# Kernel tuning notes

Measured on AMD Instinct MI355X. Metric: run time of the kernel, lower is better.

The kernel has to match this reference:

```python
import jax, jax.numpy as jnp
import numpy as np

N_NODES = 100000
N_EDGES = 1600000
D_IN, D_HID, D_OUT = 128, 128, 64


def gcn_conv(x, src, dst, deg_inv_sqrt, W, b, n_nodes):
    # PyG GCNConv (normalize=True, add_self_loops already folded into src/dst/deg):
    # out = scatter_add( d^{-1/2}[src] * d^{-1/2}[dst] * (x @ W)[src] ) + b
    h = x @ W                                    # [N, d_out]
    norm = deg_inv_sqrt[src] * deg_inv_sqrt[dst]  # [E+N]
    msg = h[src] * norm[:, None]                  # [E+N, d_out] (edge gather)
    out = jax.ops.segment_sum(msg, dst, num_segments=n_nodes)
    return out + b


def _augment(edge_index, n_nodes):
    # add self-loops and compute symmetric-normalization degrees (in-degree at dst)
    loop = jnp.arange(n_nodes, dtype=edge_index.dtype)
    src = jnp.concatenate([edge_index[0], loop])
    dst = jnp.concatenate([edge_index[1], loop])
    deg = jax.ops.segment_sum(jnp.ones_like(dst, dtype=jnp.float32), dst,
                              num_segments=n_nodes)
    deg_inv_sqrt = jnp.where(deg > 0, jax.lax.rsqrt(jnp.maximum(deg, 1.0)), 0.0)
    return src, dst, deg_inv_sqrt


def setup_inputs() -> dict:
    key = jax.random.key(0)
    k1, k2, k3, k4 = jax.random.split(key, 4)
    x = jax.random.normal(k1, (N_NODES, D_IN), dtype=jnp.float32)
    edge_index = jax.random.randint(k2, (2, N_EDGES), 0, N_NODES, dtype=jnp.int32)
    s = 1.0 / np.sqrt(D_IN)
    W1 = jax.random.uniform(k3, (D_IN, D_HID), dtype=jnp.float32, minval=-s, maxval=s)
    b1 = jnp.zeros((D_HID,), dtype=jnp.float32)
    s2 = 1.0 / np.sqrt(D_HID)
    W2 = jax.random.uniform(k4, (D_HID, D_OUT), dtype=jnp.float32, minval=-s2, maxval=s2)
    b2 = jnp.zeros((D_OUT,), dtype=jnp.float32)
    return {"x": x, "edge_index": edge_index, "W1": W1, "b1": b1, "W2": W2, "b2": b2}


def reference(x, edge_index, W1, b1, W2, b2):
    n_nodes = x.shape[0]
    src, dst, dinv = _augment(edge_index, n_nodes)
    h = gcn_conv(x, src, dst, dinv, W1, b1, n_nodes)
    h = jax.nn.relu(h)
    # dropout is identity in eval mode (F.dropout with training=False)
    out = gcn_conv(h, src, dst, dinv, W2, b2, n_nodes)
    return out
```

## Files before the change

kernel.cpp:

```cpp
#include <hip/hip_runtime.h>

typedef unsigned int uint;
typedef unsigned short ushort;
typedef __attribute__((ext_vector_type(8))) short short8v;
typedef __attribute__((ext_vector_type(4))) float f32x4;

#define NBMAX 512
#define BSHIFT 8

__device__ __forceinline__ ushort f2bf(float f) {
    uint u = __float_as_uint(f);
    u += 0x7fffu + ((u >> 16) & 1u);
    return (ushort)(u >> 16);
}


__global__ void bucket_hist(const int* __restrict__ dst, int* __restrict__ bcnt,
                            int E, int nbk) {
    __shared__ int s[NBMAX];
    int t = threadIdx.x;
    for (int i = t; i < nbk; i += 256) s[i] = 0;
    __syncthreads();
    int i0 = blockIdx.x * 4096 + t;
#pragma unroll
    for (int k = 0; k < 16; ++k) {
        int i = i0 + k * 256;
        if (i < E) atomicAdd(&s[dst[i] >> BSHIFT], 1);
    }
    __syncthreads();
    for (int i = t; i < nbk; i += 256) if (s[i] > 0) atomicAdd(&bcnt[i], s[i]);
}

__global__ void bucket_scan(const int* __restrict__ bcnt, int* __restrict__ bstart,
                            int* __restrict__ bcur, int nbk) {
    __shared__ int s[512];
    int t = threadIdx.x;
    int v = (t < nbk) ? bcnt[t] : 0;
    s[t] = v;
    __syncthreads();
    for (int o = 1; o < 512; o <<= 1) {
        int tv = (t >= o) ? s[t - o] : 0;
        __syncthreads();
        s[t] += tv;
        __syncthreads();
    }
    if (t < nbk) {
        int ex = s[t] - v;
        bstart[t] = ex;
        bcur[t] = ex;
    }
}

__global__ void bucket_scatter(const int* __restrict__ src, const int* __restrict__ dst,
                               int* __restrict__ bcur, int* __restrict__ tsw, int E) {
    __shared__ int cnt[NBMAX];
    __shared__ int base[NBMAX];
    int t = threadIdx.x;
    for (int i = t; i < NBMAX; i += 256) cnt[i] = 0;
    __syncthreads();
    int i0 = blockIdx.x * 4096 + t;
    int p_[16], b_[16], r_[16];
#pragma unroll
    for (int k = 0; k < 16; ++k) {
        int i = i0 + k * 256;
        if (i < E) {
            int s = src[i], d = dst[i];
            int bb = d >> BSHIFT;
            b_[k] = bb;
            p_[k] = s | ((d & ((1 << BSHIFT) - 1)) << 17);
            r_[k] = atomicAdd(&cnt[bb], 1);
        } else {
            b_[k] = -1;
        }
    }
    __syncthreads();
    for (int i = t; i < NBMAX; i += 256) if (cnt[i] > 0) base[i] = atomicAdd(&bcur[i], cnt[i]);
    __syncthreads();
#pragma unroll
    for (int k = 0; k < 16; ++k) {
        if (b_[k] >= 0) {
            int p = base[b_[k]] + r_[k];
            tsw[p] = p_[k];
        }
    }
}

__global__ void sort_bucket(const int* __restrict__ tsw, const int* __restrict__ bstart,
                            float* __restrict__ dinv, int* __restrict__ rp,
                            int* __restrict__ edata, int N, int E, int nbk) {
    __shared__ int cnt[256];
    __shared__ int cursor[256];
    int b = blockIdx.x;
    int t = threadIdx.x;
    int estart = bstart[b];
    int eend = (b + 1 < nbk) ? bstart[b + 1] : E;

    cnt[t] = 0;
    __syncthreads();
    for (int i = estart + t; i < eend; i += 256) {
        atomicAdd(&cnt[(uint)tsw[i] >> 17], 1);
    }
    __syncthreads();

    int node = (b << BSHIFT) + t;
    int self = (node < N) ? 1 : 0;
    int deg = cnt[t];
    int v = deg + self;
    cursor[t] = v;
    __syncthreads();
    for (int o = 1; o < 256; o <<= 1) {
        int tv = (t >= o) ? cursor[t - o] : 0;
        __syncthreads();
        cursor[t] += tv;
        __syncthreads();
    }
    int ex = cursor[t] - v;
    int gbase = estart + (b << BSHIFT);

    if (node < N) {
        dinv[node] = rsqrtf((float)(deg + 1));
        rp[node] = gbase + ex;
        edata[gbase + ex] = node;
    }
    if (b == nbk - 1 && t == 0) rp[N] = E + N;
    cursor[t] = ex + self;
    __syncthreads();

    for (int i = estart + t; i < eend; i += 256) {
        uint rec = (uint)tsw[i];
        int pos = gbase + atomicAdd(&cursor[rec >> 17], 1);
        edata[pos] = (int)(rec & 0x1FFFFu);
    }
}

__global__ void zero_row(ushort* __restrict__ Hz, int len) {
    int i = threadIdx.x;
    if (i < len) Hz[i] = 0;
}


__global__ void prep_w(const float* __restrict__ W1, const float* __restrict__ W2,
                       ushort* __restrict__ Wt1s, ushort* __restrict__ Wt2s) {
    int t = blockIdx.x * 256 + threadIdx.x;
    int total = gridDim.x * 256;
    for (int idx = t; idx < 128 * 128; idx += total) {
        int nn = idx >> 7, kk = idx & 127;
        uint byte = (uint)nn * 256u + (uint)kk * 2u;
        byte ^= (uint)((nn & 7) << 4);
        Wt1s[byte >> 1] = f2bf(W1[kk * 128 + nn]);
    }
    for (int idx = t; idx < 64 * 128; idx += total) {
        int nn = idx >> 7, kk = idx & 127;
        uint byte = (uint)nn * 256u + (uint)kk * 2u;
        byte ^= (uint)((nn & 7) << 4);
        Wt2s[byte >> 1] = f2bf(W2[kk * 64 + nn]);
    }
}


template <int NCOLS, bool IN_BF16>
__launch_bounds__(256)
__global__ void gemm_mfma(const void* __restrict__ Xv, const ushort* __restrict__ Wimg,
                          ushort* __restrict__ H, const float* __restrict__ dinv, int n) {
    constexpr int NT = NCOLS / 16;
    __shared__ ushort sW[NCOLS * 128];
    {
        const uint4* src = (const uint4*)Wimg;
        uint4* dst = (uint4*)sW;
        constexpr int NV = NCOLS * 128 * 2 / 16;
        for (int i = threadIdx.x; i < NV; i += 256) dst[i] = src[i];
    }
    __syncthreads();

    const int w  = threadIdx.x >> 6;
    const int l  = threadIdx.x & 63;
    const int lm = l & 15, lk = l >> 4;
    const int row_base = blockIdx.x * 128 + w * 32;

    f32x4 acc[2][NT];
#pragma unroll
    for (int mt = 0; mt < 2; ++mt)
#pragma unroll
        for (int nt = 0; nt < NT; ++nt) {
            f32x4 z = {0.f, 0.f, 0.f, 0.f};
            acc[mt][nt] = z;
        }

    int r0 = row_base + lm;
    int r1 = row_base + 16 + lm;
    int r0c = r0 < n ? r0 : n - 1;
    int r1c = r1 < n ? r1 : n - 1;

#pragma unroll
    for (int kb = 0; kb < 4; ++kb) {
        short8v a0, a1;
        if constexpr (IN_BF16) {
            const ushort* X = (const ushort*)Xv;
            a0 = *(const short8v*)(X + (size_t)r0c * 128 + kb * 32 + lk * 8);
            a1 = *(const short8v*)(X + (size_t)r1c * 128 + kb * 32 + lk * 8);
        } else {
            const float* X = (const float*)Xv;
            const float* p0 = X + (size_t)r0c * 128 + kb * 32 + lk * 8;
            const float* p1 = X + (size_t)r1c * 128 + kb * 32 + lk * 8;
            float4 u0 = *(const float4*)p0;
            float4 v0 = *(const float4*)(p0 + 4);
            float4 u1 = *(const float4*)p1;
            float4 v1 = *(const float4*)(p1 + 4);
            a0[0] = (short)f2bf(u0.x); a0[1] = (short)f2bf(u0.y);
            a0[2] = (short)f2bf(u0.z); a0[3] = (short)f2bf(u0.w);
            a0[4] = (short)f2bf(v0.x); a0[5] = (short)f2bf(v0.y);
            a0[6] = (short)f2bf(v0.z); a0[7] = (short)f2bf(v0.w);
            a1[0] = (short)f2bf(u1.x); a1[1] = (short)f2bf(u1.y);
            a1[2] = (short)f2bf(u1.z); a1[3] = (short)f2bf(u1.w);
            a1[4] = (short)f2bf(v1.x); a1[5] = (short)f2bf(v1.y);
            a1[6] = (short)f2bf(v1.z); a1[7] = (short)f2bf(v1.w);
        }
#pragma unroll
        for (int nt = 0; nt < NT; ++nt) {
            int nn = nt * 16 + lm;
            uint byte = (uint)nn * 256u + (uint)kb * 64u + (uint)lk * 16u;
            byte ^= (uint)((nn & 7) << 4);
            short8v b = *(const short8v*)((const char*)sW + byte);
            acc[0][nt] = __builtin_amdgcn_mfma_f32_16x16x32_bf16(a0, b, acc[0][nt], 0, 0, 0);
            acc[1][nt] = __builtin_amdgcn_mfma_f32_16x16x32_bf16(a1, b, acc[1][nt], 0, 0, 0);
        }
    }

    float dvs[2][4];
#pragma unroll
    for (int mt = 0; mt < 2; ++mt)
#pragma unroll
        for (int r = 0; r < 4; ++r) {
            int row = row_base + mt * 16 + lk * 4 + r;
            dvs[mt][r] = (row < n) ? dinv[row] : 0.f;
        }
#pragma unroll
    for (int mt = 0; mt < 2; ++mt)
#pragma unroll
        for (int nt = 0; nt < NT; ++nt)
#pragma unroll
            for (int r = 0; r < 4; ++r) {
                int row = row_base + mt * 16 + lk * 4 + r;
                if (row < n) H[(size_t)row * NCOLS + nt * 16 + lm] = f2bf(acc[mt][nt][r] * dvs[mt][r]);
            }
}


template <bool RELU>
__launch_bounds__(256)
__global__ void agg128(const ushort* __restrict__ H, const int* __restrict__ rp,
                       const int* __restrict__ edata, const float* __restrict__ dinv,
                       const float* __restrict__ bias, ushort* __restrict__ out, int N) {
    int gw = (blockIdx.x * 256 + threadIdx.x) >> 6;
    int lane = threadIdx.x & 63;
    if (gw >= N) return;
    const int h = lane >> 5, c = lane & 31;
    int e = rp[gw], end = rp[gw + 1];
    float a0 = 0.f, a1 = 0.f, a2 = 0.f, a3 = 0.f;

    for (; e < end; e += 32) {
        int md = N;
        if (lane < 32 && e + lane < end) md = edata[e + lane];
#pragma unroll
        for (int j = 0; j < 16; ++j) {
            int si = __shfl(md, 2 * j + h);
            uint2 hv = *(const uint2*)&H[(size_t)si * 128 + c * 4];
            a0 += __uint_as_float(hv.x << 16);
            a1 += __uint_as_float(hv.x & 0xffff0000u);
            a2 += __uint_as_float(hv.y << 16);
            a3 += __uint_as_float(hv.y & 0xffff0000u);
        }
    }
    a0 += __shfl_xor(a0, 32); a1 += __shfl_xor(a1, 32);
    a2 += __shfl_xor(a2, 32); a3 += __shfl_xor(a3, 32);
    if (h == 0) {
        float dg = dinv[gw];
        float4 bv = *(const float4*)&bias[c * 4];
        a0 = dg * a0 + bv.x; a1 = dg * a1 + bv.y;
        a2 = dg * a2 + bv.z; a3 = dg * a3 + bv.w;
        if (RELU) {
            a0 = fmaxf(a0, 0.f); a1 = fmaxf(a1, 0.f);
            a2 = fmaxf(a2, 0.f); a3 = fmaxf(a3, 0.f);
        }
        uint2 pk;
        pk.x = (uint)f2bf(a0) | ((uint)f2bf(a1) << 16);
        pk.y = (uint)f2bf(a2) | ((uint)f2bf(a3) << 16);
        *(uint2*)&out[(size_t)gw * 128 + c * 4] = pk;
    }
}

__launch_bounds__(256)
__global__ void agg64(const ushort* __restrict__ H, const int* __restrict__ rp,
                      const int* __restrict__ edata, const float* __restrict__ dinv,
                      const float* __restrict__ bias, float* __restrict__ out, int N) {
    int gw = (blockIdx.x * 256 + threadIdx.x) >> 6;
    int lane = threadIdx.x & 63;
    if (gw >= N) return;
    const int q = lane >> 4, c = lane & 15;
    int e = rp[gw], end = rp[gw + 1];
    float a0 = 0.f, a1 = 0.f, a2 = 0.f, a3 = 0.f;

    for (; e < end; e += 32) {
        int md = N;
        if (lane < 32 && e + lane < end) md = edata[e + lane];
#pragma unroll
        for (int j = 0; j < 8; ++j) {
            int si = __shfl(md, 4 * j + q);
            uint2 hv = *(const uint2*)&H[(size_t)si * 64 + c * 4];
            a0 += __uint_as_float(hv.x << 16);
            a1 += __uint_as_float(hv.x & 0xffff0000u);
            a2 += __uint_as_float(hv.y << 16);
            a3 += __uint_as_float(hv.y & 0xffff0000u);
        }
    }
    a0 += __shfl_xor(a0, 16); a0 += __shfl_xor(a0, 32);
    a1 += __shfl_xor(a1, 16); a1 += __shfl_xor(a1, 32);
    a2 += __shfl_xor(a2, 16); a2 += __shfl_xor(a2, 32);
    a3 += __shfl_xor(a3, 16); a3 += __shfl_xor(a3, 32);
    if (q == 0) {
        float dg = dinv[gw];
        float4 bv = *(const float4*)&bias[c * 4];
        a0 = dg * a0 + bv.x; a1 = dg * a1 + bv.y;
        a2 = dg * a2 + bv.z; a3 = dg * a3 + bv.w;
        *(float4*)&out[(size_t)gw * 64 + c * 4] = make_float4(a0, a1, a2, a3);
    }
}

__global__ void zero_out(float* __restrict__ out, int n) {
    int i = blockIdx.x * 256 + threadIdx.x;
    if (i < n) out[i] = 0.f;
}


extern "C" void kernel_launch(void* const* d_in, const int* in_sizes, int n_in,
                              void* d_out, int out_size, void* d_ws, size_t ws_size,
                              hipStream_t stream) {
    const float* x  = (const float*)d_in[0];
    const int*   ei = (const int*)d_in[1];
    const float* W1 = (const float*)d_in[2];
    const float* b1 = (const float*)d_in[3];
    const float* W2 = (const float*)d_in[4];
    const float* b2 = (const float*)d_in[5];
    float* out = (float*)d_out;

    const int N = in_sizes[0] / 128;
    const int E = in_sizes[1] / 2;
    const int* srcp = ei;
    const int* dstp = ei + E;

    char* base = (char*)d_ws;
    size_t off = 0;
    auto alloc = [&](size_t bytes) -> void* {
        void* p = base + off;
        off += (bytes + 15) & ~(size_t)15;
        return p;
    };
    ushort* H1    = (ushort*)alloc((size_t)(N + 1) * 128 * 2);
    ushort* A1    = (ushort*)alloc((size_t)N * 128 * 2);
    ushort* Wt1s  = (ushort*)alloc(128 * 128 * 2);
    ushort* Wt2s  = (ushort*)alloc(64 * 128 * 2);
    float*  dinv  = (float*)alloc((size_t)N * 4);
    int*    rp    = (int*)alloc((size_t)(N + 1) * 4);
    int*    bcnt  = (int*)alloc(NBMAX * 4);
    int*    bstart= (int*)alloc(NBMAX * 4);
    int*    bcur  = (int*)alloc(NBMAX * 4);
    int*    edata = (int*)alloc((size_t)(E + N) * 4);
    ushort* H2    = H1;

    int* tsw = (int*)A1;

    int nbk = (N + (1 << BSHIFT) - 1) >> BSHIFT;
    if (off > ws_size || (size_t)E * 4 > (size_t)N * 256 || N > (1 << 17) || nbk > NBMAX) {
        zero_out<<<(out_size + 255) / 256, 256, 0, stream>>>(out, out_size);
        return;
    }
    int nchunk = (E + 4095) / 4096;

    hipMemsetAsync(bcnt, 0, NBMAX * sizeof(int), stream);
    bucket_hist<<<nchunk, 256, 0, stream>>>(dstp, bcnt, E, nbk);
    bucket_scan<<<1, 512, 0, stream>>>(bcnt, bstart, bcur, nbk);
    bucket_scatter<<<nchunk, 256, 0, stream>>>(srcp, dstp, bcur, tsw, E);
    sort_bucket<<<nbk, 256, 0, stream>>>(tsw, bstart, dinv, rp, edata, N, E, nbk);
    zero_row<<<1, 128, 0, stream>>>(H1 + (size_t)N * 128, 128);
    prep_w<<<32, 256, 0, stream>>>(W1, W2, Wt1s, Wt2s);

    gemm_mfma<128, false><<<(N + 127) / 128, 256, 0, stream>>>(x, Wt1s, H1, dinv, N);
    agg128<true><<<(N + 3) / 4, 256, 0, stream>>>(H1, rp, edata, dinv, b1, A1, N);
    zero_row<<<1, 64, 0, stream>>>(H2 + (size_t)N * 64, 64);
    gemm_mfma<64, true><<<(N + 127) / 128, 256, 0, stream>>>(A1, Wt2s, H2, dinv, N);
    agg64<<<(N + 3) / 4, 256, 0, stream>>>(H2, rp, edata, dinv, b2, out, N);
}
```

Before: 216.1 us.

## Assign one node per half-wave/quarter-wave in aggregation and fold zero-row into GEMM

Aggregation kernels now map one destination node to 32 lanes (agg128) or 16 lanes (agg64) instead of a full wavefront, processing 16 edges per iteration, which removes the cross-lane reduction shuffles and the idle half/three-quarters of lanes at the store stage. With average degree near 17, this trims padded gather work per node. The padding zero-row writes move into the GEMM kernels, dropping two tiny kernel launches. Risk: divergence between nodes sharing a wave with different degrees, so the wave runs as long as its highest-degree node.

```diff
diff --git a/kernel.cpp b/kernel.cpp
--- a/kernel.cpp
+++ b/kernel.cpp
@@ -133,11 +133,6 @@
     }
 }
 
-__global__ void zero_row(ushort* __restrict__ Hz, int len) {
-    int i = threadIdx.x;
-    if (i < len) Hz[i] = 0;
-}
-
 
 __global__ void prep_w(const float* __restrict__ W1, const float* __restrict__ W2,
                        ushort* __restrict__ Wt1s, ushort* __restrict__ Wt2s) {
@@ -163,6 +158,7 @@
 __global__ void gemm_mfma(const void* __restrict__ Xv, const ushort* __restrict__ Wimg,
                           ushort* __restrict__ H, const float* __restrict__ dinv, int n) {
     constexpr int NT = NCOLS / 16;
+    if (blockIdx.x == 0 && threadIdx.x < NCOLS) H[(size_t)n * NCOLS + threadIdx.x] = 0;
     __shared__ ushort sW[NCOLS * 128];
     {
         const uint4* src = (const uint4*)Wimg;
@@ -251,19 +247,23 @@
 __global__ void agg128(const ushort* __restrict__ H, const int* __restrict__ rp,
                        const int* __restrict__ edata, const float* __restrict__ dinv,
                        const float* __restrict__ bias, ushort* __restrict__ out, int N) {
-    int gw = (blockIdx.x * 256 + threadIdx.x) >> 6;
-    int lane = threadIdx.x & 63;
-    if (gw >= N) return;
-    const int h = lane >> 5, c = lane & 31;
-    int e = rp[gw], end = rp[gw + 1];
+    const int lane = threadIdx.x & 63;
+    const int half = lane >> 5;
+    const int c = lane & 31;
+    const int node = blockIdx.x * 8 + ((threadIdx.x >> 6) << 1) + half;
+    if (node >= N) return;
+    int e = rp[node], end = rp[node + 1];
     float a0 = 0.f, a1 = 0.f, a2 = 0.f, a3 = 0.f;
 
-    for (; e < end; e += 32) {
+    for (; e < end; e += 16) {
         int md = N;
-        if (lane < 32 && e + lane < end) md = edata[e + lane];
+        if (c < 16) {
+            int idx = e + c;
+            if (idx < end) md = edata[idx];
+        }
 #pragma unroll
         for (int j = 0; j < 16; ++j) {
-            int si = __shfl(md, 2 * j + h);
+            int si = __shfl(md, (half << 5) + j);
             uint2 hv = *(const uint2*)&H[(size_t)si * 128 + c * 4];
             a0 += __uint_as_float(hv.x << 16);
             a1 += __uint_as_float(hv.x & 0xffff0000u);
@@ -271,41 +271,38 @@
             a3 += __uint_as_float(hv.y & 0xffff0000u);
         }
     }
-    a0 += __shfl_xor(a0, 32); a1 += __shfl_xor(a1, 32);
-    a2 += __shfl_xor(a2, 32); a3 += __shfl_xor(a3, 32);
-    if (h == 0) {
-        float dg = dinv[gw];
-        float4 bv = *(const float4*)&bias[c * 4];
-        a0 = dg * a0 + bv.x; a1 = dg * a1 + bv.y;
-        a2 = dg * a2 + bv.z; a3 = dg * a3 + bv.w;
-        if (RELU) {
-            a0 = fmaxf(a0, 0.f); a1 = fmaxf(a1, 0.f);
-            a2 = fmaxf(a2, 0.f); a3 = fmaxf(a3, 0.f);
-        }
-        uint2 pk;
-        pk.x = (uint)f2bf(a0) | ((uint)f2bf(a1) << 16);
-        pk.y = (uint)f2bf(a2) | ((uint)f2bf(a3) << 16);
-        *(uint2*)&out[(size_t)gw * 128 + c * 4] = pk;
-    }
+    float dg = dinv[node];
+    float4 bv = *(const float4*)&bias[c * 4];
+    a0 = dg * a0 + bv.x; a1 = dg * a1 + bv.y;
+    a2 = dg * a2 + bv.z; a3 = dg * a3 + bv.w;
+    if (RELU) {
+        a0 = fmaxf(a0, 0.f); a1 = fmaxf(a1, 0.f);
+        a2 = fmaxf(a2, 0.f); a3 = fmaxf(a3, 0.f);
+    }
+    uint2 pk;
+    pk.x = (uint)f2bf(a0) | ((uint)f2bf(a1) << 16);
+    pk.y = (uint)f2bf(a2) | ((uint)f2bf(a3) << 16);
+    *(uint2*)&out[(size_t)node * 128 + c * 4] = pk;
 }
 
 __launch_bounds__(256)
 __global__ void agg64(const ushort* __restrict__ H, const int* __restrict__ rp,
                       const int* __restrict__ edata, const float* __restrict__ dinv,
                       const float* __restrict__ bias, float* __restrict__ out, int N) {
-    int gw = (blockIdx.x * 256 + threadIdx.x) >> 6;
-    int lane = threadIdx.x & 63;
-    if (gw >= N) return;
-    const int q = lane >> 4, c = lane & 15;
-    int e = rp[gw], end = rp[gw + 1];
+    const int lane = threadIdx.x & 63;
+    const int qb = lane & 48;
+    const int c = lane & 15;
+    const int node = blockIdx.x * 16 + (threadIdx.x >> 4);
+    if (node >= N) return;
+    int e = rp[node], end = rp[node + 1];
     float a0 = 0.f, a1 = 0.f, a2 = 0.f, a3 = 0.f;
 
-    for (; e < end; e += 32) {
-        int md = N;
-        if (lane < 32 && e + lane < end) md = edata[e + lane];
-#pragma unroll
-        for (int j = 0; j < 8; ++j) {
-            int si = __shfl(md, 4 * j + q);
+    for (; e < end; e += 16) {
+        int idx = e + c;
+        int md = (idx < end) ? edata[idx] : N;
+#pragma unroll
+        for (int j = 0; j < 16; ++j) {
+            int si = __shfl(md, qb + j);
             uint2 hv = *(const uint2*)&H[(size_t)si * 64 + c * 4];
             a0 += __uint_as_float(hv.x << 16);
             a1 += __uint_as_float(hv.x & 0xffff0000u);
@@ -313,17 +310,11 @@
             a3 += __uint_as_float(hv.y & 0xffff0000u);
         }
     }
-    a0 += __shfl_xor(a0, 16); a0 += __shfl_xor(a0, 32);
-    a1 += __shfl_xor(a1, 16); a1 += __shfl_xor(a1, 32);
-    a2 += __shfl_xor(a2, 16); a2 += __shfl_xor(a2, 32);
-    a3 += __shfl_xor(a3, 16); a3 += __shfl_xor(a3, 32);
-    if (q == 0) {
-        float dg = dinv[gw];
-        float4 bv = *(const float4*)&bias[c * 4];
-        a0 = dg * a0 + bv.x; a1 = dg * a1 + bv.y;
-        a2 = dg * a2 + bv.z; a3 = dg * a3 + bv.w;
-        *(float4*)&out[(size_t)gw * 64 + c * 4] = make_float4(a0, a1, a2, a3);
-    }
+    float dg = dinv[node];
+    float4 bv = *(const float4*)&bias[c * 4];
+    a0 = dg * a0 + bv.x; a1 = dg * a1 + bv.y;
+    a2 = dg * a2 + bv.z; a3 = dg * a3 + bv.w;
+    *(float4*)&out[(size_t)node * 64 + c * 4] = make_float4(a0, a1, a2, a3);
 }
 
 __global__ void zero_out(float* __restrict__ out, int n) {
@@ -381,12 +372,10 @@
     bucket_scan<<<1, 512, 0, stream>>>(bcnt, bstart, bcur, nbk);
     bucket_scatter<<<nchunk, 256, 0, stream>>>(srcp, dstp, bcur, tsw, E);
     sort_bucket<<<nbk, 256, 0, stream>>>(tsw, bstart, dinv, rp, edata, N, E, nbk);
-    zero_row<<<1, 128, 0, stream>>>(H1 + (size_t)N * 128, 128);
     prep_w<<<32, 256, 0, stream>>>(W1, W2, Wt1s, Wt2s);
 
     gemm_mfma<128, false><<<(N + 127) / 128, 256, 0, stream>>>(x, Wt1s, H1, dinv, N);
-    agg128<true><<<(N + 3) / 4, 256, 0, stream>>>(H1, rp, edata, dinv, b1, A1, N);
-    zero_row<<<1, 64, 0, stream>>>(H2 + (size_t)N * 64, 64);
+    agg128<true><<<(N + 7) / 8, 256, 0, stream>>>(H1, rp, edata, dinv, b1, A1, N);
     gemm_mfma<64, true><<<(N + 127) / 128, 256, 0, stream>>>(A1, Wt2s, H2, dinv, N);
-    agg64<<<(N + 3) / 4, 256, 0, stream>>>(H2, rp, edata, dinv, b2, out, N);
-}
+    agg64<<<(N + 15) / 16, 256, 0, stream>>>(H2, rp, edata, dinv, b2, out, N);
+}
```

Result: faster. 201.9 us (-6.5%).
